# Optimization experiments

Measured on AMD Instinct MI355X. Metric: run time of the kernel, lower is better.

Reference implementation:

```python
import jax, jax.numpy as jnp
import numpy as np

EPS = 1e-8  # torch F.cosine_similarity clamps norms at eps=1e-8


def setup_inputs() -> dict:
    key = jax.random.key(0)
    k1, k2 = jax.random.split(key)
    fp_pred = jax.random.uniform(k1, (1024, 4096), dtype=jnp.float32)
    fp_cand = jax.random.uniform(k2, (16384, 4096), dtype=jnp.float32)
    return {"fp_pred": fp_pred, "fp_cand": fp_cand}


def reference(fp_pred, fp_cand):
    # Cosine similarity between every (pred, cand) pair, matching
    # F.cosine_similarity semantics: dot(a,b) / (max(|a|,eps)*max(|b|,eps)).
    # Expressed as normalized GEMM instead of the (N*M, K) expand+reduce.
    pred_norm = jnp.maximum(jnp.linalg.norm(fp_pred, axis=-1, keepdims=True), EPS)
    cand_norm = jnp.maximum(jnp.linalg.norm(fp_cand, axis=-1, keepdims=True), EPS)
    a = fp_pred / pred_norm  # (N, K)
    b = fp_cand / cand_norm  # (M, K)
    scores = jnp.einsum("nk,mk->nm", a, b)  # (N, M)
    return scores
```

## Files before the change

### kernel.cpp

```cpp
#include <hip/hip_runtime.h>
#include <stdint.h>


#define KDIM 4096
#define NPROD 3

typedef __attribute__((ext_vector_type(4))) float f32x4;
typedef __attribute__((ext_vector_type(8))) short bf16x8;
typedef __attribute__((ext_vector_type(4))) unsigned short u16x4;

typedef const __attribute__((address_space(1))) void as1_const_void;
typedef __attribute__((address_space(3))) void as3_void;

__device__ __forceinline__ unsigned short f32_bf16_rne(float f) {
  union { float f; uint32_t u; } c; c.f = f;
  uint32_t u = c.u;
  u += 0x7fffu + ((u >> 16) & 1u);
  return (unsigned short)(u >> 16);
}
__device__ __forceinline__ float bf16_f32(unsigned short h) {
  union { uint32_t u; float f; } c; c.u = ((uint32_t)h) << 16;
  return c.f;
}

__device__ __forceinline__ float row_inv_norm(const f32x4 v[4], int t) {
  float s = 0.f;
#pragma unroll
  for (int j = 0; j < 4; ++j)
#pragma unroll
    for (int e = 0; e < 4; ++e) s += v[j][e] * v[j][e];
#pragma unroll
  for (int off = 32; off > 0; off >>= 1) s += __shfl_down(s, off, 64);
  __shared__ float red[4];
  if ((t & 63) == 0) red[t >> 6] = s;
  __syncthreads();
  const float tot = red[0] + red[1] + red[2] + red[3];
  return 1.0f / fmaxf(sqrtf(tot), 1e-8f);
}

__global__ __launch_bounds__(256) void normsplit_kernel(
    const float* __restrict__ pred, const float* __restrict__ cand,
    unsigned short* __restrict__ Ahi, unsigned short* __restrict__ Alo,
    unsigned short* __restrict__ Bhi, unsigned short* __restrict__ Blo,
    int n_pred) {
  const int row = blockIdx.x;
  const int t = threadIdx.x;
  const float* src;
  unsigned short *hi, *lo;
  int r;
  if (row < n_pred) { r = row;          src = pred; hi = Ahi; lo = Alo; }
  else              { r = row - n_pred; src = cand; hi = Bhi; lo = Blo; }

  const f32x4* p = (const f32x4*)(src + (size_t)r * KDIM);
  f32x4 v[4];
#pragma unroll
  for (int j = 0; j < 4; ++j) v[j] = p[t + 256 * j];
  const float inv = row_inv_norm(v, t);

  u16x4* hq = (u16x4*)(hi + (size_t)r * KDIM);
  u16x4* lq = (u16x4*)(lo + (size_t)r * KDIM);
#pragma unroll
  for (int j = 0; j < 4; ++j) {
    u16x4 h, l;
#pragma unroll
    for (int e = 0; e < 4; ++e) {
      float x = v[j][e] * inv;
      unsigned short hb = f32_bf16_rne(x);
      float resid = x - bf16_f32(hb);
      h[e] = hb;
      l[e] = f32_bf16_rne(resid);
    }
    hq[t + 256 * j] = h;
    lq[t + 256 * j] = l;
  }
}

__global__ __launch_bounds__(256) void norms_kernel(
    const float* __restrict__ pred, const float* __restrict__ cand,
    float* __restrict__ inv_out, int n_pred) {
  const int row = blockIdx.x;
  const int t = threadIdx.x;
  const float* src = (row < n_pred) ? pred + (size_t)row * KDIM
                                    : cand + (size_t)(row - n_pred) * KDIM;
  const f32x4* p = (const f32x4*)src;
  f32x4 v[4];
#pragma unroll
  for (int j = 0; j < 4; ++j) v[j] = p[t + 256 * j];
  const float inv = row_inv_norm(v, t);
  if (t == 0) inv_out[row] = inv;
}

__device__ __forceinline__ void frag_offsets_wm(int lane, int wm, int wn,
                                                int a_off[4], int b_off[4]) {
  const int cc = lane >> 4;
#pragma unroll
  for (int m = 0; m < 4; ++m) {
    const int rr = wm + m * 16 + (lane & 15);
    a_off[m] = rr * 64 + ((cc ^ ((rr >> 1) & 3)) << 4);
  }
#pragma unroll
  for (int n = 0; n < 4; ++n) {
    const int rr = wn + n * 16 + (lane & 15);
    b_off[n] = rr * 64 + ((cc ^ ((rr >> 1) & 3)) << 4);
  }
}

__device__ __forceinline__ int xcd_swizzle(int id, int nwg) {
  if ((nwg & 7) == 0) {
    const int cpx = nwg >> 3;
    id = (id & 7) * cpx + (id >> 3);
  }
  return id;
}

#define BUF_SZ   49152
#define A_LO_OFF 16384
#define B_HI_OFF 32768
#define B_LO_OFF 40960

__global__ __launch_bounds__(512, 2) void gemm_x3_256_kernel(
    const unsigned short* __restrict__ Ahi, const unsigned short* __restrict__ Alo,
    const unsigned short* __restrict__ Bhi, const unsigned short* __restrict__ Blo,
    float* __restrict__ out, int M, int N) {
  __shared__ __align__(16) char lds[2 * BUF_SZ];
  const int tid = threadIdx.x;
  const int lane = tid & 63;
  const int wave = tid >> 6;

  const int id = xcd_swizzle(blockIdx.x, gridDim.x);
  const int mblocks = M >> 8;
  const int bm = id % mblocks;
  const int bn = id / mblocks;
  const size_t row0 = (size_t)bm * 256;
  const size_t col0 = (size_t)bn * 128;

  const unsigned short *gAh[2], *gAl[2], *gBh, *gBl;
  int loffA[2];
#pragma unroll
  for (int s = 0; s < 2; ++s) {
    const int p = s * 8192 + tid * 16;
    const int rr = p >> 6;
    const int cch = (p >> 4) & 3;
    const int e = (cch ^ ((rr >> 1) & 3)) * 8;
    gAh[s] = Ahi + (row0 + rr) * KDIM + e;
    gAl[s] = Alo + (row0 + rr) * KDIM + e;
    loffA[s] = s * 8192 + wave * 1024;
  }
  {
    const int p = tid * 16;
    const int rr = p >> 6;
    const int cch = (p >> 4) & 3;
    const int e = (cch ^ ((rr >> 1) & 3)) * 8;
    gBh = Bhi + (col0 + rr) * KDIM + e;
    gBl = Blo + (col0 + rr) * KDIM + e;
  }
  const int loffB = wave * 1024;

  const int wm = (wave >> 1) * 64;
  const int wn = (wave & 1) * 64;
  int a_off[4], b_off[4];
  frag_offsets_wm(lane, wm, wn, a_off, b_off);

  auto stage = [&](int sb, int kt) {
#pragma unroll
    for (int s = 0; s < 2; ++s) {
      __builtin_amdgcn_global_load_lds((as1_const_void*)(gAh[s] + kt),
          (as3_void*)(lds + sb + loffA[s]), 16, 0, 0);
      __builtin_amdgcn_global_load_lds((as1_const_void*)(gAl[s] + kt),
          (as3_void*)(lds + sb + A_LO_OFF + loffA[s]), 16, 0, 0);
    }
    __builtin_amdgcn_global_load_lds((as1_const_void*)(gBh + kt),
        (as3_void*)(lds + sb + B_HI_OFF + loffB), 16, 0, 0);
    __builtin_amdgcn_global_load_lds((as1_const_void*)(gBl + kt),
        (as3_void*)(lds + sb + B_LO_OFF + loffB), 16, 0, 0);
  };

  f32x4 acc[4][4] = {};

  stage(0, 0);
  __syncthreads();
  int pb = 0;

#pragma unroll 1
  for (int kt = 0; kt < KDIM; kt += 32) {
    if (kt + 32 < KDIM) stage(pb ^ BUF_SZ, kt + 32);

    bf16x8 fah[4], fal[4], fbh[4], fbl[4];
#pragma unroll
    for (int m = 0; m < 4; ++m) {
      fah[m] = *(const bf16x8*)(lds + pb + a_off[m]);
      fal[m] = *(const bf16x8*)(lds + pb + A_LO_OFF + a_off[m]);
    }
#pragma unroll
    for (int n = 0; n < 4; ++n) {
      fbh[n] = *(const bf16x8*)(lds + pb + B_HI_OFF + b_off[n]);
      fbl[n] = *(const bf16x8*)(lds + pb + B_LO_OFF + b_off[n]);
    }
#pragma unroll
    for (int m = 0; m < 4; ++m)
#pragma unroll
      for (int n = 0; n < 4; ++n) {
        acc[m][n] = __builtin_amdgcn_mfma_f32_16x16x32_bf16(fah[m], fbh[n], acc[m][n], 0, 0, 0);
        acc[m][n] = __builtin_amdgcn_mfma_f32_16x16x32_bf16(fal[m], fbh[n], acc[m][n], 0, 0, 0);
        acc[m][n] = __builtin_amdgcn_mfma_f32_16x16x32_bf16(fah[m], fbl[n], acc[m][n], 0, 0, 0);
      }

    __syncthreads();
    pb ^= BUF_SZ;
  }

  const int orow = (lane >> 4) * 4;
  const int ocol = lane & 15;
#pragma unroll
  for (int m = 0; m < 4; ++m)
#pragma unroll
    for (int n = 0; n < 4; ++n) {
      const size_t cbase = col0 + wn + n * 16 + ocol;
#pragma unroll
      for (int q = 0; q < 4; ++q) {
        const size_t rr = row0 + wm + m * 16 + orow + q;
        out[rr * (size_t)N + cbase] = acc[m][n][q];
      }
    }
}

__global__ __launch_bounds__(256, 2) void gemm_x3_kernel(
    const unsigned short* __restrict__ Ahi, const unsigned short* __restrict__ Alo,
    const unsigned short* __restrict__ Bhi, const unsigned short* __restrict__ Blo,
    float* __restrict__ out, int M, int N) {
  __shared__ unsigned short sAhi[128 * 32], sAlo[128 * 32],
                            sBhi[128 * 32], sBlo[128 * 32];
  const int tid = threadIdx.x;
  const int lane = tid & 63;
  const int wave = tid >> 6;

  const int id = xcd_swizzle(blockIdx.x, gridDim.x);
  const int mblocks = M >> 7;
  const int bm = id % mblocks;
  const int bn = id / mblocks;
  const size_t row0 = (size_t)bm * 128;
  const size_t col0 = (size_t)bn * 128;

  const unsigned short *gAh[2], *gAl[2], *gBh[2], *gBl[2];
  int loff_[2];
#pragma unroll
  for (int it = 0; it < 2; ++it) {
    const int p = it * 4096 + wave * 1024 + lane * 16;
    const int rr = p >> 6;
    const int cch = (p >> 4) & 3;
    const int e = (cch ^ ((rr >> 1) & 3)) * 8;
    gAh[it] = Ahi + (row0 + rr) * KDIM + e;
    gAl[it] = Alo + (row0 + rr) * KDIM + e;
    gBh[it] = Bhi + (col0 + rr) * KDIM + e;
    gBl[it] = Blo + (col0 + rr) * KDIM + e;
    loff_[it] = it * 4096 + wave * 1024;
  }

  const int wm = (wave >> 1) * 64;
  const int wn = (wave & 1) * 64;
  int a_off[4], b_off[4];
  frag_offsets_wm(lane, wm, wn, a_off, b_off);

  f32x4 acc[4][4] = {};

#pragma unroll 1
  for (int kt = 0; kt < KDIM; kt += 32) {
#pragma unroll
    for (int it = 0; it < 2; ++it) {
      __builtin_amdgcn_global_load_lds((as1_const_void*)(gAh[it] + kt),
                                       (as3_void*)((char*)sAhi + loff_[it]), 16, 0, 0);
      __builtin_amdgcn_global_load_lds((as1_const_void*)(gBh[it] + kt),
                                       (as3_void*)((char*)sBhi + loff_[it]), 16, 0, 0);
#if NPROD >= 3
      __builtin_amdgcn_global_load_lds((as1_const_void*)(gAl[it] + kt),
                                       (as3_void*)((char*)sAlo + loff_[it]), 16, 0, 0);
      __builtin_amdgcn_global_load_lds((as1_const_void*)(gBl[it] + kt),
                                       (as3_void*)((char*)sBlo + loff_[it]), 16, 0, 0);
#endif
    }
    __syncthreads();

    bf16x8 fah[4], fbh[4];
#if NPROD >= 3
    bf16x8 fal[4], fbl[4];
#endif
#pragma unroll
    for (int m = 0; m < 4; ++m) {
      fah[m] = *(const bf16x8*)((const char*)sAhi + a_off[m]);
#if NPROD >= 3
      fal[m] = *(const bf16x8*)((const char*)sAlo + a_off[m]);
#endif
    }
#pragma unroll
    for (int n = 0; n < 4; ++n) {
      fbh[n] = *(const bf16x8*)((const char*)sBhi + b_off[n]);
#if NPROD >= 3
      fbl[n] = *(const bf16x8*)((const char*)sBlo + b_off[n]);
#endif
    }
#pragma unroll
    for (int m = 0; m < 4; ++m)
#pragma unroll
      for (int n = 0; n < 4; ++n) {
        acc[m][n] = __builtin_amdgcn_mfma_f32_16x16x32_bf16(fah[m], fbh[n], acc[m][n], 0, 0, 0);
#if NPROD >= 3
        acc[m][n] = __builtin_amdgcn_mfma_f32_16x16x32_bf16(fal[m], fbh[n], acc[m][n], 0, 0, 0);
        acc[m][n] = __builtin_amdgcn_mfma_f32_16x16x32_bf16(fah[m], fbl[n], acc[m][n], 0, 0, 0);
#endif
      }
    __syncthreads();
  }

  const int orow = (lane >> 4) * 4;
  const int ocol = lane & 15;
#pragma unroll
  for (int m = 0; m < 4; ++m)
#pragma unroll
    for (int n = 0; n < 4; ++n) {
      const size_t cbase = col0 + wn + n * 16 + ocol;
#pragma unroll
      for (int q = 0; q < 4; ++q) {
        const size_t rr = row0 + wm + m * 16 + orow + q;
        out[rr * (size_t)N + cbase] = acc[m][n][q];
      }
    }
}

__global__ __launch_bounds__(256, 2) void gemm_fly_kernel(
    const float* __restrict__ A, const float* __restrict__ B,
    const float* __restrict__ invn, float* __restrict__ out, int M, int N) {
  __shared__ unsigned short sAhi[128 * 32], sAlo[128 * 32],
                            sBhi[128 * 32], sBlo[128 * 32];
  const int tid = threadIdx.x;
  const int lane = tid & 63;
  const int wave = tid >> 6;

  const int id = xcd_swizzle(blockIdx.x, gridDim.x);
  const int mblocks = M >> 7;
  const int bm = id % mblocks;
  const int bn = id / mblocks;
  const size_t row0 = (size_t)bm * 128;
  const size_t col0 = (size_t)bn * 128;

  const int srow = tid >> 1;
  const int scol = (tid & 1) * 16;
  int w_off[2];
#pragma unroll
  for (int g = 0; g < 2; ++g) {
    const int c = (scol >> 3) + g;
    w_off[g] = srow * 64 + ((c ^ ((srow >> 1) & 3)) << 4);
  }

  const int wm = (wave >> 1) * 64;
  const int wn = (wave & 1) * 64;
  int a_off[4], b_off[4];
  frag_offsets_wm(lane, wm, wn, a_off, b_off);

  f32x4 acc[4][4] = {};

#pragma unroll 1
  for (int kt = 0; kt < KDIM; kt += 32) {
    const f32x4* pa = (const f32x4*)(A + (row0 + srow) * KDIM + kt + scol);
    const f32x4* pb = (const f32x4*)(B + (col0 + srow) * KDIM + kt + scol);
    f32x4 va[4], vb[4];
#pragma unroll
    for (int j = 0; j < 4; ++j) { va[j] = pa[j]; vb[j] = pb[j]; }

    bf16x8 ah[2], al[2], bh[2], bl[2];
#pragma unroll
    for (int g = 0; g < 2; ++g)
#pragma unroll
      for (int e = 0; e < 8; ++e) {
        float x = va[g * 2 + (e >> 2)][e & 3];
        unsigned short hb = f32_bf16_rne(x);
        ah[g][e] = (short)hb;
        al[g][e] = (short)f32_bf16_rne(x - bf16_f32(hb));
        x = vb[g * 2 + (e >> 2)][e & 3];
        hb = f32_bf16_rne(x);
        bh[g][e] = (short)hb;
        bl[g][e] = (short)f32_bf16_rne(x - bf16_f32(hb));
      }
    __syncthreads();
#pragma unroll
    for (int g = 0; g < 2; ++g) {
      *(bf16x8*)((char*)sAhi + w_off[g]) = ah[g];
      *(bf16x8*)((char*)sBhi + w_off[g]) = bh[g];
#if NPROD >= 3
      *(bf16x8*)((char*)sAlo + w_off[g]) = al[g];
      *(bf16x8*)((char*)sBlo + w_off[g]) = bl[g];
#endif
    }
    __syncthreads();

    bf16x8 fah[4], fbh[4];
#if NPROD >= 3
    bf16x8 fal[4], fbl[4];
#endif
#pragma unroll
    for (int m = 0; m < 4; ++m) {
      fah[m] = *(const bf16x8*)((const char*)sAhi + a_off[m]);
#if NPROD >= 3
      fal[m] = *(const bf16x8*)((const char*)sAlo + a_off[m]);
#endif
    }
#pragma unroll
    for (int n = 0; n < 4; ++n) {
      fbh[n] = *(const bf16x8*)((const char*)sBhi + b_off[n]);
#if NPROD >= 3
      fbl[n] = *(const bf16x8*)((const char*)sBlo + b_off[n]);
#endif
    }
#pragma unroll
    for (int m = 0; m < 4; ++m)
#pragma unroll
      for (int n = 0; n < 4; ++n) {
        acc[m][n] = __builtin_amdgcn_mfma_f32_16x16x32_bf16(fah[m], fbh[n], acc[m][n], 0, 0, 0);
#if NPROD >= 3
        acc[m][n] = __builtin_amdgcn_mfma_f32_16x16x32_bf16(fal[m], fbh[n], acc[m][n], 0, 0, 0);
        acc[m][n] = __builtin_amdgcn_mfma_f32_16x16x32_bf16(fah[m], fbl[n], acc[m][n], 0, 0, 0);
#endif
      }
  }

  const float* invP = invn;
  const float* invC = invn + M;
  const int orow = (lane >> 4) * 4;
  const int ocol = lane & 15;
#pragma unroll
  for (int m = 0; m < 4; ++m)
#pragma unroll
    for (int n = 0; n < 4; ++n) {
      const size_t cidx = col0 + wn + n * 16 + ocol;
      const float ib = invC[cidx];
#pragma unroll
      for (int q = 0; q < 4; ++q) {
        const size_t rr = row0 + wm + m * 16 + orow + q;
        out[rr * (size_t)N + cidx] = acc[m][n][q] * invP[rr] * ib;
      }
    }
}

__global__ __launch_bounds__(256) void fallback_kernel(
    const float* __restrict__ A, const float* __restrict__ B,
    float* __restrict__ out, int M, int N) {
  __shared__ float sA[32][36], sB[32][36];
  __shared__ float invA[32], invB[32];
  __shared__ float part[64][4];
  const int t = threadIdx.x;
  const int bi = blockIdx.y;
  const int bj = blockIdx.x;
  const size_t r0a = (size_t)bi * 32, r0b = (size_t)bj * 32;

  {
    const int rr = t >> 2, seg = t & 3;
    const float* src = (rr < 32) ? (A + (r0a + rr) * KDIM)
                                 : (B + (r0b + rr - 32) * KDIM);
    const f32x4* p = (const f32x4*)src;
    float s = 0.f;
    for (int i = seg * 256; i < seg * 256 + 256; ++i) {
      f32x4 v = p[i];
      s += v[0] * v[0] + v[1] * v[1] + v[2] * v[2] + v[3] * v[3];
    }
    part[rr][seg] = s;
  }
  __syncthreads();
  if (t < 64) {
    const float s = part[t][0] + part[t][1] + part[t][2] + part[t][3];
    const float inv = 1.0f / fmaxf(sqrtf(s), 1e-8f);
    if (t < 32) invA[t] = inv; else invB[t - 32] = inv;
  }
  __syncthreads();

  float acc[4] = {0.f, 0.f, 0.f, 0.f};
  const int c = t & 31;
  const int rbase = t >> 5;
  for (int kt = 0; kt < KDIM; kt += 32) {
    const int rr = t >> 3, ccc = (t & 7) * 4;
    *(f32x4*)&sA[rr][ccc] = *(const f32x4*)(A + (r0a + rr) * KDIM + kt + ccc);
    *(f32x4*)&sB[rr][ccc] = *(const f32x4*)(B + (r0b + rr) * KDIM + kt + ccc);
    __syncthreads();
#pragma unroll
    for (int kk = 0; kk < 32; ++kk) {
      const float bv = sB[c][kk];
      acc[0] += sA[rbase][kk] * bv;
      acc[1] += sA[rbase + 8][kk] * bv;
      acc[2] += sA[rbase + 16][kk] * bv;
      acc[3] += sA[rbase + 24][kk] * bv;
    }
    __syncthreads();
  }
#pragma unroll
  for (int i = 0; i < 4; ++i) {
    const int rr = rbase + 8 * i;
    out[(r0a + rr) * (size_t)N + r0b + c] = acc[i] * invA[rr] * invB[c];
  }
}

extern "C" void kernel_launch(void* const* d_in, const int* in_sizes, int n_in,
                              void* d_out, int out_size, void* d_ws, size_t ws_size,
                              hipStream_t stream) {
  const float* pred = (const float*)d_in[0];
  const float* cand = (const float*)d_in[1];
  float* out = (float*)d_out;
  const int n_pred = in_sizes[0] / KDIM;
  const int n_cand = in_sizes[1] / KDIM;
  const int n_rows = n_pred + n_cand;

  const size_t need_big = (size_t)n_rows * KDIM * 2 * 2;
  const size_t need_small = (size_t)n_rows * sizeof(float);
  const bool shapes_ok = (n_pred % 128 == 0) && (n_cand % 128 == 0) &&
                         (n_pred * KDIM == in_sizes[0]) &&
                         (n_cand * KDIM == in_sizes[1]);

  if (shapes_ok && ws_size >= need_big) {
    unsigned short* Ahi = (unsigned short*)d_ws;
    unsigned short* Alo = Ahi + (size_t)n_pred * KDIM;
    unsigned short* Bhi = Alo + (size_t)n_pred * KDIM;
    unsigned short* Blo = Bhi + (size_t)n_cand * KDIM;
    normsplit_kernel<<<n_rows, 256, 0, stream>>>(pred, cand, Ahi, Alo, Bhi, Blo,
                                                 n_pred);
    if (n_pred % 256 == 0) {
      const int nwg = (n_pred / 256) * (n_cand / 128);
      gemm_x3_256_kernel<<<nwg, 512, 0, stream>>>(Ahi, Alo, Bhi, Blo, out,
                                                  n_pred, n_cand);
    } else {
      const int nwg = (n_pred / 128) * (n_cand / 128);
      gemm_x3_kernel<<<nwg, 256, 0, stream>>>(Ahi, Alo, Bhi, Blo, out, n_pred,
                                              n_cand);
    }
  } else if (shapes_ok && ws_size >= need_small) {
    float* invn = (float*)d_ws;
    const int nwg = (n_pred / 128) * (n_cand / 128);
    norms_kernel<<<n_rows, 256, 0, stream>>>(pred, cand, invn, n_pred);
    gemm_fly_kernel<<<nwg, 256, 0, stream>>>(pred, cand, invn, out, n_pred,
                                             n_cand);
  } else {
    dim3 grid(n_cand / 32, n_pred / 32);
    fallback_kernel<<<grid, 256, 0, stream>>>(pred, cand, out, n_pred, n_cand);
  }
}
```

Before: 777.8 us.

## Drop candidate low-part split: use two bf16 products instead of three

```diff
diff --git a/kernel.cpp b/kernel.cpp
--- a/kernel.cpp
+++ b/kernel.cpp
@@ -3,7 +3,7 @@
 
 
 #define KDIM 4096
-#define NPROD 3
+#define NPROD 2
 
 typedef __attribute__((ext_vector_type(4))) float f32x4;
 typedef __attribute__((ext_vector_type(8))) short bf16x8;
@@ -23,71 +23,84 @@
   return c.f;
 }
 
-__device__ __forceinline__ float row_inv_norm(const f32x4 v[4], int t) {
-  float s = 0.f;
-#pragma unroll
-  for (int j = 0; j < 4; ++j)
-#pragma unroll
-    for (int e = 0; e < 4; ++e) s += v[j][e] * v[j][e];
-#pragma unroll
-  for (int off = 32; off > 0; off >>= 1) s += __shfl_down(s, off, 64);
-  __shared__ float red[4];
-  if ((t & 63) == 0) red[t >> 6] = s;
-  __syncthreads();
-  const float tot = red[0] + red[1] + red[2] + red[3];
-  return 1.0f / fmaxf(sqrtf(tot), 1e-8f);
-}
-
-__global__ __launch_bounds__(256) void normsplit_kernel(
+__global__ __launch_bounds__(256) void normsplit2_kernel(
     const float* __restrict__ pred, const float* __restrict__ cand,
     unsigned short* __restrict__ Ahi, unsigned short* __restrict__ Alo,
     unsigned short* __restrict__ Bhi, unsigned short* __restrict__ Blo,
-    int n_pred) {
-  const int row = blockIdx.x;
-  const int t = threadIdx.x;
+    int n_pred, int n_rows) {
+  const int lane = threadIdx.x & 63;
+  const int row = (blockIdx.x << 2) + (threadIdx.x >> 6);
+  if (row >= n_rows) return;
+
   const float* src;
   unsigned short *hi, *lo;
   int r;
-  if (row < n_pred) { r = row;          src = pred; hi = Ahi; lo = Alo; }
-  else              { r = row - n_pred; src = cand; hi = Bhi; lo = Blo; }
+  bool has_lo;
+  if (row < n_pred) {
+    r = row; src = pred; hi = Ahi; lo = Alo; has_lo = true;
+  } else {
+    r = row - n_pred; src = cand; hi = Bhi; lo = Blo; has_lo = (NPROD >= 3);
+  }
 
   const f32x4* p = (const f32x4*)(src + (size_t)r * KDIM);
-  f32x4 v[4];
-#pragma unroll
-  for (int j = 0; j < 4; ++j) v[j] = p[t + 256 * j];
-  const float inv = row_inv_norm(v, t);
+  f32x4 v[16];
+  float s = 0.f;
+#pragma unroll
+  for (int j = 0; j < 16; ++j) {
+    v[j] = p[lane + 64 * j];
+#pragma unroll
+    for (int e = 0; e < 4; ++e) s += v[j][e] * v[j][e];
+  }
+#pragma unroll
+  for (int off = 32; off > 0; off >>= 1) s += __shfl_xor(s, off, 64);
+  const float inv = 1.0f / fmaxf(sqrtf(s), 1e-8f);
 
   u16x4* hq = (u16x4*)(hi + (size_t)r * KDIM);
-  u16x4* lq = (u16x4*)(lo + (size_t)r * KDIM);
-#pragma unroll
-  for (int j = 0; j < 4; ++j) {
-    u16x4 h, l;
-#pragma unroll
-    for (int e = 0; e < 4; ++e) {
-      float x = v[j][e] * inv;
-      unsigned short hb = f32_bf16_rne(x);
-      float resid = x - bf16_f32(hb);
-      h[e] = hb;
-      l[e] = f32_bf16_rne(resid);
-    }
-    hq[t + 256 * j] = h;
-    lq[t + 256 * j] = l;
+  if (has_lo) {
+    u16x4* lq = (u16x4*)(lo + (size_t)r * KDIM);
+#pragma unroll
+    for (int j = 0; j < 16; ++j) {
+      u16x4 h, l;
+#pragma unroll
+      for (int e = 0; e < 4; ++e) {
+        const float x = v[j][e] * inv;
+        const unsigned short hb = f32_bf16_rne(x);
+        h[e] = hb;
+        l[e] = f32_bf16_rne(x - bf16_f32(hb));
+      }
+      hq[lane + 64 * j] = h;
+      lq[lane + 64 * j] = l;
+    }
+  } else {
+#pragma unroll
+    for (int j = 0; j < 16; ++j) {
+      u16x4 h;
+#pragma unroll
+      for (int e = 0; e < 4; ++e) h[e] = f32_bf16_rne(v[j][e] * inv);
+      hq[lane + 64 * j] = h;
+    }
   }
 }
 
 __global__ __launch_bounds__(256) void norms_kernel(
     const float* __restrict__ pred, const float* __restrict__ cand,
-    float* __restrict__ inv_out, int n_pred) {
-  const int row = blockIdx.x;
-  const int t = threadIdx.x;
+    float* __restrict__ inv_out, int n_pred, int n_rows) {
+  const int lane = threadIdx.x & 63;
+  const int row = (blockIdx.x << 2) + (threadIdx.x >> 6);
+  if (row >= n_rows) return;
   const float* src = (row < n_pred) ? pred + (size_t)row * KDIM
                                     : cand + (size_t)(row - n_pred) * KDIM;
   const f32x4* p = (const f32x4*)src;
-  f32x4 v[4];
-#pragma unroll
-  for (int j = 0; j < 4; ++j) v[j] = p[t + 256 * j];
-  const float inv = row_inv_norm(v, t);
-  if (t == 0) inv_out[row] = inv;
+  float s = 0.f;
+#pragma unroll
+  for (int j = 0; j < 16; ++j) {
+    const f32x4 v = p[lane + 64 * j];
+#pragma unroll
+    for (int e = 0; e < 4; ++e) s += v[e] * v[e];
+  }
+#pragma unroll
+  for (int off = 32; off > 0; off >>= 1) s += __shfl_xor(s, off, 64);
+  if (lane == 0) inv_out[row] = 1.0f / fmaxf(sqrtf(s), 1e-8f);
 }
 
 __device__ __forceinline__ void frag_offsets_wm(int lane, int wm, int wn,
@@ -113,14 +126,13 @@
   return id;
 }
 
-#define BUF_SZ   49152
+#define BUF_SZ   40960
 #define A_LO_OFF 16384
 #define B_HI_OFF 32768
-#define B_LO_OFF 40960
-
-__global__ __launch_bounds__(512, 2) void gemm_x3_256_kernel(
+
+__global__ __launch_bounds__(512, 4) void gemm_x2_256_kernel(
     const unsigned short* __restrict__ Ahi, const unsigned short* __restrict__ Alo,
-    const unsigned short* __restrict__ Bhi, const unsigned short* __restrict__ Blo,
+    const unsigned short* __restrict__ Bhi,
     float* __restrict__ out, int M, int N) {
   __shared__ __align__(16) char lds[2 * BUF_SZ];
   const int tid = threadIdx.x;
@@ -134,7 +146,7 @@
   const size_t row0 = (size_t)bm * 256;
   const size_t col0 = (size_t)bn * 128;
 
-  const unsigned short *gAh[2], *gAl[2], *gBh, *gBl;
+  const unsigned short *gAh[2], *gAl[2], *gBh;
   int loffA[2];
 #pragma unroll
   for (int s = 0; s < 2; ++s) {
@@ -152,7 +164,6 @@
     const int cch = (p >> 4) & 3;
     const int e = (cch ^ ((rr >> 1) & 3)) * 8;
     gBh = Bhi + (col0 + rr) * KDIM + e;
-    gBl = Blo + (col0 + rr) * KDIM + e;
   }
   const int loffB = wave * 1024;
 
@@ -171,8 +182,6 @@
     }
     __builtin_amdgcn_global_load_lds((as1_const_void*)(gBh + kt),
         (as3_void*)(lds + sb + B_HI_OFF + loffB), 16, 0, 0);
-    __builtin_amdgcn_global_load_lds((as1_const_void*)(gBl + kt),
-        (as3_void*)(lds + sb + B_LO_OFF + loffB), 16, 0, 0);
   };
 
   f32x4 acc[4][4] = {};
@@ -185,24 +194,22 @@
   for (int kt = 0; kt < KDIM; kt += 32) {
     if (kt + 32 < KDIM) stage(pb ^ BUF_SZ, kt + 32);
 
-    bf16x8 fah[4], fal[4], fbh[4], fbl[4];
+    bf16x8 fah[4], fal[4], fbh[4];
 #pragma unroll
     for (int m = 0; m < 4; ++m) {
       fah[m] = *(const bf16x8*)(lds + pb + a_off[m]);
       fal[m] = *(const bf16x8*)(lds + pb + A_LO_OFF + a_off[m]);
     }
 #pragma unroll
-    for (int n = 0; n < 4; ++n) {
+    for (int n = 0; n < 4; ++n)
       fbh[n] = *(const bf16x8*)(lds + pb + B_HI_OFF + b_off[n]);
-      fbl[n] = *(const bf16x8*)(lds + pb + B_LO_OFF + b_off[n]);
-    }
+
 #pragma unroll
     for (int m = 0; m < 4; ++m)
 #pragma unroll
       for (int n = 0; n < 4; ++n) {
         acc[m][n] = __builtin_amdgcn_mfma_f32_16x16x32_bf16(fah[m], fbh[n], acc[m][n], 0, 0, 0);
         acc[m][n] = __builtin_amdgcn_mfma_f32_16x16x32_bf16(fal[m], fbh[n], acc[m][n], 0, 0, 0);
-        acc[m][n] = __builtin_amdgcn_mfma_f32_16x16x32_bf16(fah[m], fbl[n], acc[m][n], 0, 0, 0);
       }
 
     __syncthreads();
@@ -224,12 +231,14 @@
     }
 }
 
-__global__ __launch_bounds__(256, 2) void gemm_x3_kernel(
+__global__ __launch_bounds__(256, 2) void gemm_x2_128_kernel(
     const unsigned short* __restrict__ Ahi, const unsigned short* __restrict__ Alo,
-    const unsigned short* __restrict__ Bhi, const unsigned short* __restrict__ Blo,
+    const unsigned short* __restrict__ Bhi,
     float* __restrict__ out, int M, int N) {
-  __shared__ unsigned short sAhi[128 * 32], sAlo[128 * 32],
-                            sBhi[128 * 32], sBlo[128 * 32];
+  __shared__ unsigned short sAhi[128 * 32], sBhi[128 * 32];
+#if NPROD >= 2
+  __shared__ unsigned short sAlo[128 * 32];
+#endif
   const int tid = threadIdx.x;
   const int lane = tid & 63;
   const int wave = tid >> 6;
@@ -241,7 +250,7 @@
   const size_t row0 = (size_t)bm * 128;
   const size_t col0 = (size_t)bn * 128;
 
-  const unsigned short *gAh[2], *gAl[2], *gBh[2], *gBl[2];
+  const unsigned short *gAh[2], *gAl[2], *gBh[2];
   int loff_[2];
 #pragma unroll
   for (int it = 0; it < 2; ++it) {
@@ -252,7 +261,6 @@
     gAh[it] = Ahi + (row0 + rr) * KDIM + e;
     gAl[it] = Alo + (row0 + rr) * KDIM + e;
     gBh[it] = Bhi + (col0 + rr) * KDIM + e;
-    gBl[it] = Blo + (col0 + rr) * KDIM + e;
     loff_[it] = it * 4096 + wave * 1024;
   }
 
@@ -271,41 +279,34 @@
                                        (as3_void*)((char*)sAhi + loff_[it]), 16, 0, 0);
       __builtin_amdgcn_global_load_lds((as1_const_void*)(gBh[it] + kt),
                                        (as3_void*)((char*)sBhi + loff_[it]), 16, 0, 0);
-#if NPROD >= 3
+#if NPROD >= 2
       __builtin_amdgcn_global_load_lds((as1_const_void*)(gAl[it] + kt),
                                        (as3_void*)((char*)sAlo + loff_[it]), 16, 0, 0);
-      __builtin_amdgcn_global_load_lds((as1_const_void*)(gBl[it] + kt),
-                                       (as3_void*)((char*)sBlo + loff_[it]), 16, 0, 0);
 #endif
     }
     __syncthreads();
 
     bf16x8 fah[4], fbh[4];
-#if NPROD >= 3
-    bf16x8 fal[4], fbl[4];
+#if NPROD >= 2
+    bf16x8 fal[4];
 #endif
 #pragma unroll
     for (int m = 0; m < 4; ++m) {
       fah[m] = *(const bf16x8*)((const char*)sAhi + a_off[m]);
-#if NPROD >= 3
+#if NPROD >= 2
       fal[m] = *(const bf16x8*)((const char*)sAlo + a_off[m]);
 #endif
     }
 #pragma unroll
-    for (int n = 0; n < 4; ++n) {
+    for (int n = 0; n < 4; ++n)
       fbh[n] = *(const bf16x8*)((const char*)sBhi + b_off[n]);
-#if NPROD >= 3
-      fbl[n] = *(const bf16x8*)((const char*)sBlo + b_off[n]);
-#endif
-    }
 #pragma unroll
     for (int m = 0; m < 4; ++m)
 #pragma unroll
       for (int n = 0; n < 4; ++n) {
         acc[m][n] = __builtin_amdgcn_mfma_f32_16x16x32_bf16(fah[m], fbh[n], acc[m][n], 0, 0, 0);
-#if NPROD >= 3
+#if NPROD >= 2
         acc[m][n] = __builtin_amdgcn_mfma_f32_16x16x32_bf16(fal[m], fbh[n], acc[m][n], 0, 0, 0);
-        acc[m][n] = __builtin_amdgcn_mfma_f32_16x16x32_bf16(fah[m], fbl[n], acc[m][n], 0, 0, 0);
 #endif
       }
     __syncthreads();
@@ -329,8 +330,10 @@
 __global__ __launch_bounds__(256, 2) void gemm_fly_kernel(
     const float* __restrict__ A, const float* __restrict__ B,
     const float* __restrict__ invn, float* __restrict__ out, int M, int N) {
-  __shared__ unsigned short sAhi[128 * 32], sAlo[128 * 32],
-                            sBhi[128 * 32], sBlo[128 * 32];
+  __shared__ unsigned short sAhi[128 * 32], sBhi[128 * 32];
+#if NPROD >= 2
+  __shared__ unsigned short sAlo[128 * 32];
+#endif
   const int tid = threadIdx.x;
   const int lane = tid & 63;
   const int wave = tid >> 6;
@@ -366,7 +369,7 @@
 #pragma unroll
     for (int j = 0; j < 4; ++j) { va[j] = pa[j]; vb[j] = pb[j]; }
 
-    bf16x8 ah[2], al[2], bh[2], bl[2];
+    bf16x8 ah[2], al[2], bh[2];
 #pragma unroll
     for (int g = 0; g < 2; ++g)
 #pragma unroll
@@ -376,48 +379,40 @@
         ah[g][e] = (short)hb;
         al[g][e] = (short)f32_bf16_rne(x - bf16_f32(hb));
         x = vb[g * 2 + (e >> 2)][e & 3];
-        hb = f32_bf16_rne(x);
-        bh[g][e] = (short)hb;
-        bl[g][e] = (short)f32_bf16_rne(x - bf16_f32(hb));
+        bh[g][e] = (short)f32_bf16_rne(x);
       }
     __syncthreads();
 #pragma unroll
     for (int g = 0; g < 2; ++g) {
       *(bf16x8*)((char*)sAhi + w_off[g]) = ah[g];
       *(bf16x8*)((char*)sBhi + w_off[g]) = bh[g];
-#if NPROD >= 3
+#if NPROD >= 2
       *(bf16x8*)((char*)sAlo + w_off[g]) = al[g];
-      *(bf16x8*)((char*)sBlo + w_off[g]) = bl[g];
 #endif
     }
     __syncthreads();
 
     bf16x8 fah[4], fbh[4];
-#if NPROD >= 3
-    bf16x8 fal[4], fbl[4];
+#if NPROD >= 2
+    bf16x8 fal[4];
 #endif
 #pragma unroll
     for (int m = 0; m < 4; ++m) {
       fah[m] = *(const bf16x8*)((const char*)sAhi + a_off[m]);
-#if NPROD >= 3
+#if NPROD >= 2
       fal[m] = *(const bf16x8*)((const char*)sAlo + a_off[m]);
 #endif
     }
 #pragma unroll
-    for (int n = 0; n < 4; ++n) {
+    for (int n = 0; n < 4; ++n)
       fbh[n] = *(const bf16x8*)((const char*)sBhi + b_off[n]);
-#if NPROD >= 3
-      fbl[n] = *(const bf16x8*)((const char*)sBlo + b_off[n]);
-#endif
-    }
 #pragma unroll
     for (int m = 0; m < 4; ++m)
 #pragma unroll
       for (int n = 0; n < 4; ++n) {
         acc[m][n] = __builtin_amdgcn_mfma_f32_16x16x32_bf16(fah[m], fbh[n], acc[m][n], 0, 0, 0);
-#if NPROD >= 3
+#if NPROD >= 2
         acc[m][n] = __builtin_amdgcn_mfma_f32_16x16x32_bf16(fal[m], fbh[n], acc[m][n], 0, 0, 0);
-        acc[m][n] = __builtin_amdgcn_mfma_f32_16x16x32_bf16(fah[m], fbl[n], acc[m][n], 0, 0, 0);
 #endif
       }
   }
@@ -506,7 +501,9 @@
   const int n_cand = in_sizes[1] / KDIM;
   const int n_rows = n_pred + n_cand;
 
-  const size_t need_big = (size_t)n_rows * KDIM * 2 * 2;
+  const size_t elems_big =
+      (size_t)(2 * n_pred + (NPROD >= 3 ? 2 : 1) * n_cand) * KDIM;
+  const size_t need_big = elems_big * 2;
   const size_t need_small = (size_t)n_rows * sizeof(float);
   const bool shapes_ok = (n_pred % 128 == 0) && (n_cand % 128 == 0) &&
                          (n_pred * KDIM == in_sizes[0]) &&
@@ -517,21 +514,22 @@
     unsigned short* Alo = Ahi + (size_t)n_pred * KDIM;
     unsigned short* Bhi = Alo + (size_t)n_pred * KDIM;
     unsigned short* Blo = Bhi + (size_t)n_cand * KDIM;
-    normsplit_kernel<<<n_rows, 256, 0, stream>>>(pred, cand, Ahi, Alo, Bhi, Blo,
-                                                 n_pred);
+    normsplit2_kernel<<<(n_rows + 3) / 4, 256, 0, stream>>>(
+        pred, cand, Ahi, Alo, Bhi, Blo, n_pred, n_rows);
     if (n_pred % 256 == 0) {
       const int nwg = (n_pred / 256) * (n_cand / 128);
-      gemm_x3_256_kernel<<<nwg, 512, 0, stream>>>(Ahi, Alo, Bhi, Blo, out,
+      gemm_x2_256_kernel<<<nwg, 512, 0, stream>>>(Ahi, Alo, Bhi, out,
                                                   n_pred, n_cand);
     } else {
       const int nwg = (n_pred / 128) * (n_cand / 128);
-      gemm_x3_kernel<<<nwg, 256, 0, stream>>>(Ahi, Alo, Bhi, Blo, out, n_pred,
-                                              n_cand);
+      gemm_x2_128_kernel<<<nwg, 256, 0, stream>>>(Ahi, Alo, Bhi, out,
+                                                  n_pred, n_cand);
     }
   } else if (shapes_ok && ws_size >= need_small) {
     float* invn = (float*)d_ws;
     const int nwg = (n_pred / 128) * (n_cand / 128);
-    norms_kernel<<<n_rows, 256, 0, stream>>>(pred, cand, invn, n_pred);
+    norms_kernel<<<(n_rows + 3) / 4, 256, 0, stream>>>(pred, cand, invn,
+                                                       n_pred, n_rows);
     gemm_fly_kernel<<<nwg, 256, 0, stream>>>(pred, cand, invn, out, n_pred,
                                              n_cand);
   } else {
```

Measured after the change: 623.6 us. -19.8%, faster.
